# Performance work log

Hardware: AMD Instinct MI355X
Metric: run time of the kernel (lower is better)

## Reference

```python
import jax, jax.numpy as jnp
import numpy as np
import math

H, M, N = 64, 128, 128  # volume dims (m == n required by original index math)
K_NEIGH = 9
W_WIN = 3


def build_neighbor_ids(h, n, w):
    # Periodic (wrap-around) neighbor indices, matching extract_neighbour_indices
    # with m == n. Loop order: z-major, then y, then x, offsets -1..1 for w=3.
    half = w // 2
    offs = list(range(-half, half + 1))
    zi = jnp.arange(h)[:, None, None]
    yi = jnp.arange(n)[None, :, None]
    xi = jnp.arange(n)[None, None, :]
    cols = []
    for oz in offs:
        for oy in offs:
            for ox in offs:
                idx = ((zi + oz) % h) * (n * n) + ((yi + oy) % n) * n + ((xi + ox) % n)
                cols.append(idx.reshape(-1))
    return jnp.stack(cols, axis=1).astype(jnp.int32)  # [P, w^3]


def setup_inputs() -> dict:
    key = jax.random.key(0)
    k1, _ = jax.random.split(key)
    inp = jax.random.normal(k1, (H, M, N), dtype=jnp.float32)
    ksigma = jnp.ones((1, 1, 1, 1), dtype=jnp.float32)  # nn.Parameter init to sigma_m=1.0
    return {"input": inp, "ksigma": ksigma, "k": K_NEIGH, "w": W_WIN}


def reference(input, ksigma, k, w):
    h, m, n = input.shape
    ID = build_neighbor_ids(h, n, w)               # [P, nN]
    anat = input.reshape(-1)                       # [P]
    # get_knn: absolute intensity differences to each neighbor
    dist = jnp.abs(anat[ID] - anat[:, None])       # [P, nN]
    order = jnp.argsort(dist, axis=-1, stable=True)
    sID = jnp.take_along_axis(ID, order, axis=1)   # sorted neighbor indices
    IDk = sID[:, :k]                               # [P, k] top-k nearest by intensity
    Wk = anat[IDk]                                 # [P, k] neighbor intensities (feature rows)
    # get_features: per-row std (torch.std is unbiased, ddof=1)
    sigma = jnp.std(Wk, axis=1, ddof=1)            # [P]
    sigma_safe = jnp.where(sigma == 0, 1.0, sigma)
    neigh = Wk[IDk]                                # [P, k, k] gather feature rows of knn
    diff = Wk[:, None, :] - neigh + 1e-6           # pairwise_distance eps added to diff
    norm = jnp.sqrt(jnp.sum(diff * diff, axis=-1)) # [P, k] L2 pairwise distance
    ks = ksigma.reshape(())
    logits = -jnp.square(norm / sigma_safe[:, None] / (math.sqrt(2.0) * ks))
    logits = jnp.where(sigma[:, None] == 0, 0.0, logits)  # zero row -> uniform softmax
    Kw = jax.nn.softmax(logits, axis=1)            # [P, k] normalized kernel weights
    return Kw
```

## Files before the change

### kernel.cpp

```cpp
#include <hip/hip_runtime.h>
#include <hip/hip_fp16.h>
#include <array>

constexpr int HZ   = 64;
constexpr int NN   = 128;
constexpr int P    = HZ * NN * NN;
constexpr int KSEL = 9;
constexpr int NCOL = 27;

typedef _Float16 f16x2 __attribute__((ext_vector_type(2)));

constexpr int compute_nce(int n) {
  int t = 0; while ((1 << t) < n) ++t;
  int cnt = 0;
  for (int p = 1 << (t - 1); p > 0; p >>= 1) {
    int q = 1 << (t - 1), r = 0, d = p;
    while (true) {
      for (int i = 0; i < n - d; ++i)
        if ((i & p) == r) ++cnt;
      if (q == p) break;
      d = q - p; r = p; q >>= 1;
    }
  }
  return cnt;
}
constexpr int NCE_FULL = compute_nce(NCOL);

struct CEPair { unsigned char a, b; };
constexpr std::array<CEPair, NCE_FULL> make_net() {
  std::array<CEPair, NCE_FULL> net{};
  int t = 0; while ((1 << t) < NCOL) ++t;
  int k = 0;
  for (int p = 1 << (t - 1); p > 0; p >>= 1) {
    int q = 1 << (t - 1), r = 0, d = p;
    while (true) {
      for (int i = 0; i < NCOL - d; ++i)
        if ((i & p) == r) {
          net[k].a = (unsigned char)i;
          net[k].b = (unsigned char)(i + d);
          ++k;
        }
      if (q == p) break;
      d = q - p; r = p; q >>= 1;
    }
  }
  return net;
}
constexpr auto FULLNET = make_net();

constexpr int count_pruned() {
  bool needed[NCOL] = {};
  for (int i = 0; i < KSEL; ++i) needed[i] = true;
  int cnt = 0;
  for (int e = NCE_FULL - 1; e >= 0; --e) {
    const int a = FULLNET[e].a, b = FULLNET[e].b;
    if (needed[a] || needed[b]) { needed[a] = true; needed[b] = true; ++cnt; }
  }
  return cnt;
}
constexpr int NCE = count_pruned();

constexpr std::array<CEPair, NCE> make_pruned() {
  bool needed[NCOL] = {};
  for (int i = 0; i < KSEL; ++i) needed[i] = true;
  std::array<bool, NCE_FULL> keep{};
  for (int e = NCE_FULL - 1; e >= 0; --e) {
    const int a = FULLNET[e].a, b = FULLNET[e].b;
    if (needed[a] || needed[b]) { keep[e] = true; needed[a] = true; needed[b] = true; }
  }
  std::array<CEPair, NCE> out{};
  int k = 0;
  for (int e = 0; e < NCE_FULL; ++e) if (keep[e]) out[k++] = FULLNET[e];
  return out;
}
constexpr auto NET = make_pruned();

typedef const __attribute__((address_space(1))) unsigned GU;
typedef __attribute__((address_space(3))) unsigned LU;

__device__ __forceinline__ void g2l16(const void* g, void* l) {
  __builtin_amdgcn_global_load_lds((GU*)g, (LU*)l, 16, 0, 0);
}

constexpr int TXW = 40;
constexpr int TPR = 30;

__global__ __launch_bounds__(256) void topk11(
    const float* __restrict__ anat,
    uint4* __restrict__ rowsA,
    unsigned* __restrict__ rowsB0,
    unsigned* __restrict__ rowsB1) {
  __shared__ float in_t[TPR * TXW];
  const int tid = threadIdx.x;

  const int blk = blockIdx.x;
  const int swz = ((blk & 7) << 9) | (blk >> 3);
  const int z    = swz >> 6;
  const int rest = swz & 63;
  const int y0   = ((rest >> 2) & 15) << 3;
  const int x0   = (rest & 3) << 5;
  const int xl   = tid & 31;
  const int yl   = tid >> 5;

  #pragma unroll
  for (int s = 0; s < 2; ++s) {
    const unsigned q = (unsigned)(s * 256 + tid);
    if (q < 300u) {
      const unsigned p = q / 10u;
      const unsigned t = q - 10u * p;
      const unsigned zi = p / 10u;
      const unsigned yi = p - 10u * zi;
      const int zz = (z + (int)zi - 1) & (HZ - 1);
      const int yy = (y0 + (int)yi - 1) & (NN - 1);
      const int xb = (x0 - 4 + 4 * (int)t) & (NN - 1);
      g2l16(&anat[(zz << 14) | (yy << 7) | xb], &in_t[q * 4]);
    }
  }
  __syncthreads();

  const float center = in_t[(1 * 10 + (yl + 1)) * TXW + 3 + (xl + 1)];

  unsigned long long key[NCOL];
  #pragma unroll
  for (int c = 0; c < NCOL; ++c) {
    const int czi = c / 9, cyi = (c / 3) % 3, cxi = c % 3;
    const float v = in_t[(czi * 10 + (yl + cyi)) * TXW + 3 + xl + cxi];
    const unsigned vb = __float_as_uint(v);
    const unsigned db = __float_as_uint(v - center) & 0x7fffffffu;
    const unsigned lo32 = ((unsigned)c << 27) | (vb >> 5);
    key[c] = ((unsigned long long)db << 32) | lo32;
  }

  #pragma unroll
  for (int e = 0; e < NCE; ++e) {
    const int a = NET[e].a, b = NET[e].b;
    const double ka = __builtin_bit_cast(double, key[a]);
    const double kb = __builtin_bit_cast(double, key[b]);
    key[a] = __builtin_bit_cast(unsigned long long, fmin(ka, kb));
    key[b] = __builtin_bit_cast(unsigned long long, fmax(ka, kb));
  }

  unsigned od[4] = {0, 0, 0, 0};
  unsigned h8 = 0, lo = 0, hi = 0;
  #pragma unroll
  for (int s = 0; s < KSEL; ++s) {
    const unsigned kl = (unsigned)key[s];
    const unsigned c  = (kl >> 27) & 31u;
    const unsigned vbits = (kl & 0x07ffffffu) << 5;
    const unsigned hb = (unsigned)__half_as_ushort(__float2half(__uint_as_float(vbits)));
    if (s < 8) od[s >> 1] |= hb << ((s & 1) * 16);
    else       h8 = hb;
    if (s < 6) lo |= c << (5 * s);
    else       hi |= c << (5 * (s - 6));
  }

  const unsigned vb = (unsigned)((z << 14) | ((y0 + yl) << 7) | (x0 + xl));
  rowsA[vb]  = make_uint4(od[0], od[1], od[2], od[3]);
  rowsB0[vb] = h8 | (hi << 16);
  rowsB1[vb] = lo;
}

constexpr int WPR  = 40;
constexpr int WTA  = WPR * 34;
constexpr int WTB  = WPR * TXW;

__global__ __launch_bounds__(256, 4) void weights11(
    const uint4* __restrict__ rowsA,
    const unsigned* __restrict__ rowsB0,
    const unsigned* __restrict__ rowsB1,
    const float* __restrict__ ksig,
    float* __restrict__ out) {
  __shared__ unsigned lds[WTA * 4 + WTB];
  unsigned* tA  = lds;
  unsigned* tB0 = lds + WTA * 4;
  const int tid = threadIdx.x;

  const int blk = blockIdx.x;
  const int swz = ((blk & 7) << 8) | (blk >> 3);
  const int zp   = swz >> 6;
  const int rest = swz & 63;
  const int y0   = ((rest >> 2) & 15) << 3;
  const int x0   = (rest & 3) << 5;
  const int xl   = tid & 31;
  const int yl   = tid >> 5;
  const int z0   = zp << 1;

  const unsigned vbA = (unsigned)((z0 << 14) | ((y0 + yl) << 7) | (x0 + xl));
  const unsigned low[2] = { rowsB1[vbA], rowsB1[vbA + (1u << 14)] };

  #pragma unroll
  for (int s = 0; s < 6; ++s) {
    const unsigned q = (unsigned)(s * 256 + tid);
    if (q < (unsigned)WTA) {
      const unsigned p = q / 34u;
      const unsigned r = q - 34u * p;
      const unsigned zi = p / 10u;
      const unsigned yi = p - 10u * zi;
      const int zz = (z0 + (int)zi - 1) & (HZ - 1);
      const int yy = (y0 + (int)yi - 1) & (NN - 1);
      const int xg = (x0 - 1 + (int)r) & (NN - 1);
      g2l16(&rowsA[(zz << 14) | (yy << 7) | xg], &tA[q * 4]);
    }
  }
  #pragma unroll
  for (int s = 0; s < 2; ++s) {
    const unsigned q = (unsigned)(s * 256 + tid);
    if (q < 400u) {
      const unsigned p = q / 10u;
      const unsigned t = q - 10u * p;
      const unsigned zi = p / 10u;
      const unsigned yi = p - 10u * zi;
      const int zz = (z0 + (int)zi - 1) & (HZ - 1);
      const int yy = (y0 + (int)yi - 1) & (NN - 1);
      const int xb = (x0 - 4 + 4 * (int)t) & (NN - 1);
      g2l16(&rowsB0[(zz << 14) | (yy << 7) | xb], &tB0[q * 4]);
    }
  }
  __syncthreads();

  const float ks = ksig[0];
  const _Float16 epsh = (_Float16)1e-6f;
  const f16x2 eps2 = {epsh, epsh};

  float res[2][9];

  #pragma unroll 2
  for (int vz = 0; vz < 2; ++vz) {
    const unsigned lo = low[vz];
    const int planeO = 1 + vz;

    const int prO = planeO * 10 + (yl + 1);
    const uint4 a = *(const uint4*)&tA[(prO * 34 + (xl + 1)) * 4];
    const unsigned b0 = tB0[prO * TXW + (xl + 4)];
    f16x2 wh[5];
    wh[0] = __builtin_bit_cast(f16x2, a.x);
    wh[1] = __builtin_bit_cast(f16x2, a.y);
    wh[2] = __builtin_bit_cast(f16x2, a.z);
    wh[3] = __builtin_bit_cast(f16x2, a.w);
    wh[4] = __builtin_bit_cast(f16x2, b0 & 0xffffu);
    const unsigned hi = b0 >> 16;

    int rA[KSEL], rB[KSEL];
    #pragma unroll
    for (int j = 0; j < KSEL; ++j) {
      const unsigned c = (j < 6) ? ((lo >> (5 * j)) & 31u)
                                 : ((hi >> (5 * (j - 6))) & 31u);
      const unsigned czi = (c * 57u) >> 9;
      const unsigned rem = c - 9u * czi;
      const unsigned cyi = (rem * 11u) >> 5;
      const unsigned cxi = rem - 3u * cyi;
      const int pr = (vz + (int)czi) * 10 + (yl + (int)cyi);
      rA[j] = pr * 34 + (xl + (int)cxi);
      rB[j] = pr * TXW + (xl + (int)cxi + 3);
    }
    uint4 na[KSEL];
    unsigned nb[KSEL];
    #pragma unroll
    for (int j = 0; j < KSEL; ++j) {
      na[j] = *(const uint4*)&tA[rA[j] * 4];
      nb[j] = tB0[rB[j]];
    }

    float ws[KSEL];
    #pragma unroll
    for (int l = 0; l < KSEL; ++l) ws[l] = (float)wh[l >> 1][l & 1];
    float mean = 0.f;
    #pragma unroll
    for (int l = 0; l < KSEL; ++l) mean += ws[l];
    mean *= (1.0f / 9.0f);
    float var = 0.f;
    #pragma unroll
    for (int l = 0; l < KSEL; ++l) { const float t = ws[l] - mean; var += t * t; }
    var *= (1.0f / 8.0f);
    const float sigma = sqrtf(var);

    const float inv2 = (sigma == 0.f)
        ? 0.f
        : 1.4426950408889634f / (2.0f * ks * ks * sigma * sigma);

    float logit[KSEL];
    #pragma unroll
    for (int j = 0; j < KSEL; ++j) {
      const f16x2 nh0 = __builtin_bit_cast(f16x2, na[j].x);
      const f16x2 nh1 = __builtin_bit_cast(f16x2, na[j].y);
      const f16x2 nh2 = __builtin_bit_cast(f16x2, na[j].z);
      const f16x2 nh3 = __builtin_bit_cast(f16x2, na[j].w);
      const f16x2 nh4 = __builtin_bit_cast(f16x2, nb[j] & 0xffffu);
      float s = 0.f;
      f16x2 dd;
      dd = (wh[0] - nh0) + eps2; s = __builtin_amdgcn_fdot2(dd, dd, s, false);
      dd = (wh[1] - nh1) + eps2; s = __builtin_amdgcn_fdot2(dd, dd, s, false);
      dd = (wh[2] - nh2) + eps2; s = __builtin_amdgcn_fdot2(dd, dd, s, false);
      dd = (wh[3] - nh3) + eps2; s = __builtin_amdgcn_fdot2(dd, dd, s, false);
      dd = (wh[4] - nh4) + eps2; s = __builtin_amdgcn_fdot2(dd, dd, s, false);
      logit[j] = -s * inv2;
    }

    float mx = logit[0];
    #pragma unroll
    for (int j = 1; j < KSEL; ++j) mx = fmaxf(mx, logit[j]);
    float sum = 0.f;
    float e[KSEL];
    #pragma unroll
    for (int j = 0; j < KSEL; ++j) { e[j] = exp2f(logit[j] - mx); sum += e[j]; }
    const float rs = 1.0f / sum;
    #pragma unroll
    for (int j = 0; j < KSEL; ++j) res[vz][j] = e[j] * rs;
  }

  __syncthreads();
  float* tf = (float*)lds;
  #pragma unroll 2
  for (int vz = 0; vz < 2; ++vz)
    #pragma unroll
    for (int j = 0; j < KSEL; ++j)
      tf[(vz * 256 + tid) * KSEL + j] = res[vz][j];
  __syncthreads();

  const float4* tf4 = (const float4*)lds;
  #pragma unroll
  for (int s = 0; s < 5; ++s) {
    const unsigned q = (unsigned)(s * 256 + tid);
    if (q < 1152u) {
      const unsigned row = q / 72u;
      const unsigned f   = q - row * 72u;
      const int zz = z0 + (int)(row >> 3);
      const int yr = (int)(row & 7u);
      const unsigned vb = (unsigned)((zz << 14) | ((y0 + yr) << 7) | x0);
      ((float4*)out)[(size_t)(vb >> 2) * 9 + f] = tf4[row * 72 + f];
    }
  }
}

extern "C" void kernel_launch(void* const* d_in, const int* in_sizes, int n_in,
                              void* d_out, int out_size, void* d_ws, size_t ws_size,
                              hipStream_t stream) {
  const float* anat = (const float*)d_in[0];
  const float* ksig = (const float*)d_in[1];
  uint4* rowsA     = (uint4*)d_ws;
  unsigned* rowsB0 = (unsigned*)((char*)d_ws + (size_t)16 * P);
  unsigned* rowsB1 = (unsigned*)((char*)d_ws + (size_t)20 * P);

  topk11<<<P / 256, 256, 0, stream>>>(anat, rowsA, rowsB0, rowsB1);
  weights11<<<P / 512, 256, 0, stream>>>(rowsA, rowsB0, rowsB1, ksig, (float*)d_out);
}
```

Before: 109.2 us.

## Fuse top-k and weight kernels with halo recomputation in LDS

Merges the two-pass pipeline into one kernel. Each 512-thread block loads a wider input halo, runs the 27-element sorting network for every voxel of a 6x10x34 halo region into LDS, then computes the softmax weights for a 4x8x32 output tile from LDS. This removes the global write and read-back of the packed per-voxel neighbour rows and one kernel launch. In exchange it runs the expensive sort about twice per output voxel and needs about 64KB of LDS per block, which limits occupancy.

```diff
diff --git a/kernel.cpp b/kernel.cpp
--- a/kernel.cpp
+++ b/kernel.cpp
@@ -9,6 +9,13 @@
 constexpr int NCOL = 27;
 
 typedef _Float16 f16x2 __attribute__((ext_vector_type(2)));
+
+constexpr int CZ = 4, CY = 8, CX = 32;
+constexpr int RZ = 6, RY = 10, RX = 34;
+constexpr int NROWS = RZ * RY * RX;
+constexpr int IZ = 8, IY = 12, IXW = 40;
+constexpr int NIN = IZ * IY * IXW;
+constexpr int NIN16 = IZ * IY * (IXW / 4);
 
 constexpr int compute_nce(int n) {
   int t = 0; while ((1 << t) < n) ++t;
@@ -82,141 +89,98 @@
   __builtin_amdgcn_global_load_lds((GU*)g, (LU*)l, 16, 0, 0);
 }
 
-constexpr int TXW = 40;
-constexpr int TPR = 30;
-
-__global__ __launch_bounds__(256) void topk11(
+__global__ __launch_bounds__(512) void buildk_fused(
     const float* __restrict__ anat,
-    uint4* __restrict__ rowsA,
-    unsigned* __restrict__ rowsB0,
-    unsigned* __restrict__ rowsB1) {
-  __shared__ float in_t[TPR * TXW];
+    const float* __restrict__ ksig,
+    float* __restrict__ out) {
+  __shared__ unsigned lds[NROWS * 6 + NIN];
+  unsigned* tA  = lds;
+  unsigned* tB0 = lds + NROWS * 4;
+  unsigned* tB1 = tB0 + NROWS;
+  float*    in_t = (float*)(tB1 + NROWS);
+
   const int tid = threadIdx.x;
 
   const int blk = blockIdx.x;
-  const int swz = ((blk & 7) << 9) | (blk >> 3);
-  const int z    = swz >> 6;
+  const int swz = ((blk & 7) << 7) | (blk >> 3);
+  const int zt   = swz >> 6;
   const int rest = swz & 63;
   const int y0   = ((rest >> 2) & 15) << 3;
   const int x0   = (rest & 3) << 5;
-  const int xl   = tid & 31;
-  const int yl   = tid >> 5;
+  const int z0   = zt << 2;
 
   #pragma unroll
   for (int s = 0; s < 2; ++s) {
-    const unsigned q = (unsigned)(s * 256 + tid);
-    if (q < 300u) {
+    const unsigned q = (unsigned)(s * 512 + tid);
+    if (q < (unsigned)NIN16) {
       const unsigned p = q / 10u;
       const unsigned t = q - 10u * p;
-      const unsigned zi = p / 10u;
-      const unsigned yi = p - 10u * zi;
-      const int zz = (z + (int)zi - 1) & (HZ - 1);
-      const int yy = (y0 + (int)yi - 1) & (NN - 1);
+      const unsigned iz = p / 12u;
+      const unsigned iy = p - 12u * iz;
+      const int zz = (z0 + (int)iz - 2) & (HZ - 1);
+      const int yy = (y0 + (int)iy - 2) & (NN - 1);
       const int xb = (x0 - 4 + 4 * (int)t) & (NN - 1);
       g2l16(&anat[(zz << 14) | (yy << 7) | xb], &in_t[q * 4]);
     }
   }
   __syncthreads();
 
-  const float center = in_t[(1 * 10 + (yl + 1)) * TXW + 3 + (xl + 1)];
-
-  unsigned long long key[NCOL];
-  #pragma unroll
-  for (int c = 0; c < NCOL; ++c) {
-    const int czi = c / 9, cyi = (c / 3) % 3, cxi = c % 3;
-    const float v = in_t[(czi * 10 + (yl + cyi)) * TXW + 3 + xl + cxi];
-    const unsigned vb = __float_as_uint(v);
-    const unsigned db = __float_as_uint(v - center) & 0x7fffffffu;
-    const unsigned lo32 = ((unsigned)c << 27) | (vb >> 5);
-    key[c] = ((unsigned long long)db << 32) | lo32;
-  }
-
-  #pragma unroll
-  for (int e = 0; e < NCE; ++e) {
-    const int a = NET[e].a, b = NET[e].b;
-    const double ka = __builtin_bit_cast(double, key[a]);
-    const double kb = __builtin_bit_cast(double, key[b]);
-    key[a] = __builtin_bit_cast(unsigned long long, fmin(ka, kb));
-    key[b] = __builtin_bit_cast(unsigned long long, fmax(ka, kb));
-  }
-
-  unsigned od[4] = {0, 0, 0, 0};
-  unsigned h8 = 0, lo = 0, hi = 0;
-  #pragma unroll
-  for (int s = 0; s < KSEL; ++s) {
-    const unsigned kl = (unsigned)key[s];
-    const unsigned c  = (kl >> 27) & 31u;
-    const unsigned vbits = (kl & 0x07ffffffu) << 5;
-    const unsigned hb = (unsigned)__half_as_ushort(__float2half(__uint_as_float(vbits)));
-    if (s < 8) od[s >> 1] |= hb << ((s & 1) * 16);
-    else       h8 = hb;
-    if (s < 6) lo |= c << (5 * s);
-    else       hi |= c << (5 * (s - 6));
-  }
-
-  const unsigned vb = (unsigned)((z << 14) | ((y0 + yl) << 7) | (x0 + xl));
-  rowsA[vb]  = make_uint4(od[0], od[1], od[2], od[3]);
-  rowsB0[vb] = h8 | (hi << 16);
-  rowsB1[vb] = lo;
-}
-
-constexpr int WPR  = 40;
-constexpr int WTA  = WPR * 34;
-constexpr int WTB  = WPR * TXW;
-
-__global__ __launch_bounds__(256, 4) void weights11(
-    const uint4* __restrict__ rowsA,
-    const unsigned* __restrict__ rowsB0,
-    const unsigned* __restrict__ rowsB1,
-    const float* __restrict__ ksig,
-    float* __restrict__ out) {
-  __shared__ unsigned lds[WTA * 4 + WTB];
-  unsigned* tA  = lds;
-  unsigned* tB0 = lds + WTA * 4;
-  const int tid = threadIdx.x;
-
-  const int blk = blockIdx.x;
-  const int swz = ((blk & 7) << 8) | (blk >> 3);
-  const int zp   = swz >> 6;
-  const int rest = swz & 63;
-  const int y0   = ((rest >> 2) & 15) << 3;
-  const int x0   = (rest & 3) << 5;
-  const int xl   = tid & 31;
-  const int yl   = tid >> 5;
-  const int z0   = zp << 1;
-
-  const unsigned vbA = (unsigned)((z0 << 14) | ((y0 + yl) << 7) | (x0 + xl));
-  const unsigned low[2] = { rowsB1[vbA], rowsB1[vbA + (1u << 14)] };
-
-  #pragma unroll
-  for (int s = 0; s < 6; ++s) {
-    const unsigned q = (unsigned)(s * 256 + tid);
-    if (q < (unsigned)WTA) {
-      const unsigned p = q / 34u;
-      const unsigned r = q - 34u * p;
-      const unsigned zi = p / 10u;
-      const unsigned yi = p - 10u * zi;
-      const int zz = (z0 + (int)zi - 1) & (HZ - 1);
-      const int yy = (y0 + (int)yi - 1) & (NN - 1);
-      const int xg = (x0 - 1 + (int)r) & (NN - 1);
-      g2l16(&rowsA[(zz << 14) | (yy << 7) | xg], &tA[q * 4]);
-    }
-  }
-  #pragma unroll
-  for (int s = 0; s < 2; ++s) {
-    const unsigned q = (unsigned)(s * 256 + tid);
-    if (q < 400u) {
-      const unsigned p = q / 10u;
-      const unsigned t = q - 10u * p;
-      const unsigned zi = p / 10u;
-      const unsigned yi = p - 10u * zi;
-      const int zz = (z0 + (int)zi - 1) & (HZ - 1);
-      const int yy = (y0 + (int)yi - 1) & (NN - 1);
-      const int xb = (x0 - 4 + 4 * (int)t) & (NN - 1);
-      g2l16(&rowsB0[(zz << 14) | (yy << 7) | xb], &tB0[q * 4]);
+  #pragma unroll 1
+  for (int s = 0; s < 4; ++s) {
+    const int r = s * 512 + tid;
+    if (r < NROWS) {
+      const unsigned ru = (unsigned)r;
+      const unsigned rz  = ru / (unsigned)(RY * RX);
+      const unsigned rem = ru - (unsigned)(RY * RX) * rz;
+      const unsigned ry  = rem / (unsigned)RX;
+      const unsigned rx  = rem - (unsigned)RX * ry;
+
+      const float center = in_t[((rz + 1) * IY + (ry + 1)) * IXW + rx + 3];
+
+      unsigned long long key[NCOL];
+      #pragma unroll
+      for (int c = 0; c < NCOL; ++c) {
+        const int czi = c / 9, cyi = (c / 3) % 3, cxi = c % 3;
+        const float v = in_t[((rz + czi) * IY + (ry + cyi)) * IXW + rx + cxi + 2];
+        const unsigned vb = __float_as_uint(v);
+        const unsigned db = __float_as_uint(v - center) & 0x7fffffffu;
+        const unsigned lo32 = ((unsigned)c << 27) | (vb >> 5);
+        key[c] = ((unsigned long long)db << 32) | lo32;
+      }
+
+      #pragma unroll
+      for (int e = 0; e < NCE; ++e) {
+        const int a = NET[e].a, b = NET[e].b;
+        const double ka = __builtin_bit_cast(double, key[a]);
+        const double kb = __builtin_bit_cast(double, key[b]);
+        key[a] = __builtin_bit_cast(unsigned long long, fmin(ka, kb));
+        key[b] = __builtin_bit_cast(unsigned long long, fmax(ka, kb));
+      }
+
+      unsigned od[4] = {0, 0, 0, 0};
+      unsigned h8 = 0, lo = 0, hi = 0;
+      #pragma unroll
+      for (int k = 0; k < KSEL; ++k) {
+        const unsigned kl = (unsigned)key[k];
+        const unsigned c  = (kl >> 27) & 31u;
+        const unsigned vbits = (kl & 0x07ffffffu) << 5;
+        const unsigned hb = (unsigned)__half_as_ushort(__float2half(__uint_as_float(vbits)));
+        if (k < 8) od[k >> 1] |= hb << ((k & 1) * 16);
+        else       h8 = hb;
+        if (k < 6) lo |= c << (5 * k);
+        else       hi |= c << (5 * (k - 6));
+      }
+
+      *(uint4*)&tA[ru * 4] = make_uint4(od[0], od[1], od[2], od[3]);
+      tB0[ru] = h8 | (hi << 16);
+      tB1[ru] = lo;
     }
   }
   __syncthreads();
+
+  const int xl = tid & 31;
+  const int yl = (tid >> 5) & 7;
+  const int zl = tid >> 8;
 
   const float ks = ksig[0];
   const _Float16 epsh = (_Float16)1e-6f;
@@ -226,12 +190,12 @@
 
   #pragma unroll 2
   for (int vz = 0; vz < 2; ++vz) {
-    const unsigned lo = low[vz];
-    const int planeO = 1 + vz;
-
-    const int prO = planeO * 10 + (yl + 1);
-    const uint4 a = *(const uint4*)&tA[(prO * 34 + (xl + 1)) * 4];
-    const unsigned b0 = tB0[prO * TXW + (xl + 4)];
+    const int zv = 2 * zl + vz;
+
+    const int rho_own = ((zv + 1) * RY + (yl + 1)) * RX + (xl + 1);
+    const uint4 a = *(const uint4*)&tA[rho_own * 4];
+    const unsigned b0 = tB0[rho_own];
+    const unsigned lo = tB1[rho_own];
     f16x2 wh[5];
     wh[0] = __builtin_bit_cast(f16x2, a.x);
     wh[1] = __builtin_bit_cast(f16x2, a.y);
@@ -240,7 +204,7 @@
     wh[4] = __builtin_bit_cast(f16x2, b0 & 0xffffu);
     const unsigned hi = b0 >> 16;
 
-    int rA[KSEL], rB[KSEL];
+    int rho[KSEL];
     #pragma unroll
     for (int j = 0; j < KSEL; ++j) {
       const unsigned c = (j < 6) ? ((lo >> (5 * j)) & 31u)
@@ -249,16 +213,14 @@
       const unsigned rem = c - 9u * czi;
       const unsigned cyi = (rem * 11u) >> 5;
       const unsigned cxi = rem - 3u * cyi;
-      const int pr = (vz + (int)czi) * 10 + (yl + (int)cyi);
-      rA[j] = pr * 34 + (xl + (int)cxi);
-      rB[j] = pr * TXW + (xl + (int)cxi + 3);
+      rho[j] = ((zv + (int)czi) * RY + (yl + (int)cyi)) * RX + (xl + (int)cxi);
     }
     uint4 na[KSEL];
     unsigned nb[KSEL];
     #pragma unroll
     for (int j = 0; j < KSEL; ++j) {
-      na[j] = *(const uint4*)&tA[rA[j] * 4];
-      nb[j] = tB0[rB[j]];
+      na[j] = *(const uint4*)&tA[rho[j] * 4];
+      nb[j] = tB0[rho[j]];
     }
 
     float ws[KSEL];
@@ -311,17 +273,19 @@
   __syncthreads();
   float* tf = (float*)lds;
   #pragma unroll 2
-  for (int vz = 0; vz < 2; ++vz)
-    #pragma unroll
-    for (int j = 0; j < KSEL; ++j)
-      tf[(vz * 256 + tid) * KSEL + j] = res[vz][j];
+  for (int vz = 0; vz < 2; ++vz) {
+    const int zv = 2 * zl + vz;
+    const int pos = (zv << 8) + (yl << 5) + xl;
+    #pragma unroll
+    for (int j = 0; j < KSEL; ++j) tf[pos * KSEL + j] = res[vz][j];
+  }
   __syncthreads();
 
   const float4* tf4 = (const float4*)lds;
   #pragma unroll
   for (int s = 0; s < 5; ++s) {
-    const unsigned q = (unsigned)(s * 256 + tid);
-    if (q < 1152u) {
+    const unsigned q = (unsigned)(s * 512 + tid);
+    if (q < 2304u) {
       const unsigned row = q / 72u;
       const unsigned f   = q - row * 72u;
       const int zz = z0 + (int)(row >> 3);
@@ -337,10 +301,5 @@
                               hipStream_t stream) {
   const float* anat = (const float*)d_in[0];
   const float* ksig = (const float*)d_in[1];
-  uint4* rowsA     = (uint4*)d_ws;
-  unsigned* rowsB0 = (unsigned*)((char*)d_ws + (size_t)16 * P);
-  unsigned* rowsB1 = (unsigned*)((char*)d_ws + (size_t)20 * P);
-
-  topk11<<<P / 256, 256, 0, stream>>>(anat, rowsA, rowsB0, rowsB1);
-  weights11<<<P / 512, 256, 0, stream>>>(rowsA, rowsB0, rowsB1, ksig, (float*)d_out);
-}
+  buildk_fused<<<P / (CZ * CY * CX), 512, 0, stream>>>(anat, ksig, (float*)d_out);
+}
```

Measured after the change: 105.8 us. -3.1%, faster.
